# Kernel tuning notes

Measured on AMD Instinct MI355X. Metric: run time of the kernel, lower is better.

The kernel has to match this reference:

```python
import jax, jax.numpy as jnp
import numpy as np

SPATIAL = ((100, 100), (50, 50), (25, 25), (13, 13))
STARTS = [0]
for _h, _w in SPATIAL[:-1]:
    STARTS.append(STARTS[-1] + _h * _w)
L_TOTAL = sum(h * w for h, w in SPATIAL)  # 13294
D, DFFN, NL, NH, NP = 256, 1024, 4, 8, 4
DH = D // NH
EPS = 1e-5


def _ln(x, g, b):
    mu = x.mean(-1, keepdims=True)
    var = ((x - mu) ** 2).mean(-1, keepdims=True)
    return (x - mu) * jax.lax.rsqrt(var + EPS) * g + b


def _bilinear(v_l, x, y, H, W):
    # v_l: [B,NH,H*W,DH]; x,y: [B,NH,Q*NP] pixel coords (grid_sample align_corners=False, zero padding)
    x0f = jnp.floor(x); y0f = jnp.floor(y)
    lx, ly = x - x0f, y - y0f
    x0 = x0f.astype(jnp.int32); y0 = y0f.astype(jnp.int32)
    acc = 0.0
    for dx, dy, w in ((0, 0, (1 - lx) * (1 - ly)), (1, 0, lx * (1 - ly)),
                      (0, 1, (1 - lx) * ly), (1, 1, lx * ly)):
        xi, yi = x0 + dx, y0 + dy
        valid = (xi >= 0) & (xi < W) & (yi >= 0) & (yi < H)
        idx = jnp.clip(yi, 0, H - 1) * W + jnp.clip(xi, 0, W - 1)
        g = jnp.take_along_axis(v_l, idx[..., None], axis=2)  # [B,NH,Q*NP,DH]
        acc = acc + g * (w * valid.astype(w.dtype))[..., None]
    return acc


def _msdeform(query, value_in, ref, norm_wh, Woff, boff, Wattn, battn, Wval, bval, Wout, bout):
    B, Q, _ = query.shape
    v = (value_in @ Wval + bval).reshape(B, L_TOTAL, NH, DH)
    off = (query @ Woff + boff).reshape(B, Q, NH, NL, NP, 2)
    aw = (query @ Wattn + battn).reshape(B, Q, NH, NL * NP)
    aw = jax.nn.softmax(aw, axis=-1).reshape(B, Q, NH, NL, NP)
    # normalized sampling locations in [0,1]: ref + offset / (W,H)
    loc = ref[:, :, None, :, None, :] + off / norm_wh[None, None, None, :, None, :]
    out = 0.0
    for l, (H, W) in enumerate(SPATIAL):
        s = STARTS[l]
        v_l = v[:, s:s + H * W].transpose(0, 2, 1, 3)          # [B,NH,HW,DH]
        loc_l = loc[:, :, :, l].transpose(0, 2, 1, 3, 4)       # [B,NH,Q,NP,2]
        x = (loc_l[..., 0] * W - 0.5).reshape(B, NH, Q * NP)
        y = (loc_l[..., 1] * H - 0.5).reshape(B, NH, Q * NP)
        samp = _bilinear(v_l, x, y, H, W).reshape(B, NH, Q, NP, DH)
        w_l = aw[:, :, :, l].transpose(0, 2, 1, 3)             # [B,NH,Q,NP]
        out = out + (samp * w_l[..., None]).sum(3)             # [B,NH,Q,DH]
    out = out.transpose(0, 2, 1, 3).reshape(B, Q, D)
    return out @ Wout + bout


def setup_inputs() -> dict:
    key = jax.random.key(0)
    ks = jax.random.split(key, 12)
    B = 4
    s = 0.02
    return {
        "src": jax.random.normal(ks[0], (B, L_TOTAL, D), jnp.float32),
        "pos": jax.random.normal(ks[1], (B, L_TOTAL, D), jnp.float32),
        "reference_points": jax.random.uniform(ks[2], (B, L_TOTAL, NL, 2), jnp.float32),
        "spatial_shapes": jnp.array(SPATIAL, jnp.int32),
        "level_start_index": jnp.array(STARTS, jnp.int32),
        "W_off": jax.random.normal(ks[3], (D, NH * NL * NP * 2), jnp.float32) * 0.01,
        "b_off": jax.random.normal(ks[4], (NH * NL * NP * 2,), jnp.float32) * 0.5,
        "W_attn": jax.random.normal(ks[5], (D, NH * NL * NP), jnp.float32) * s,
        "b_attn": jnp.zeros((NH * NL * NP,), jnp.float32),
        "W_val": jax.random.normal(ks[6], (D, D), jnp.float32) * s,
        "b_val": jnp.zeros((D,), jnp.float32),
        "W_out": jax.random.normal(ks[7], (D, D), jnp.float32) * s,
        "b_out": jnp.zeros((D,), jnp.float32),
        "ln_sa_g": jnp.ones((D,), jnp.float32),
        "ln_sa_b": jnp.zeros((D,), jnp.float32),
        "W1": jax.random.normal(ks[8], (D, DFFN), jnp.float32) * s,
        "b1": jnp.zeros((DFFN,), jnp.float32),
        "W2": jax.random.normal(ks[9], (DFFN, D), jnp.float32) * s,
        "b2": jnp.zeros((D,), jnp.float32),
        "ln_ff_g": jnp.ones((D,), jnp.float32),
        "ln_ff_b": jnp.zeros((D,), jnp.float32),
    }


def reference(src, pos, reference_points, spatial_shapes, level_start_index,
              W_off, b_off, W_attn, b_attn, W_val, b_val, W_out, b_out,
              ln_sa_g, ln_sa_b, W1, b1, W2, b2, ln_ff_g, ln_ff_b):
    # offset normalizer is (W, H) per level
    norm_wh = jnp.stack([spatial_shapes[:, 1], spatial_shapes[:, 0]], -1).astype(src.dtype)
    q = src + pos  # with_pos_embed
    sa = _msdeform(q, src, reference_points, norm_wh,
                   W_off, b_off, W_attn, b_attn, W_val, b_val, W_out, b_out)
    x = _ln(sa + src, ln_sa_g, ln_sa_b)          # dropout = identity (eval)
    y = jnp.maximum(x @ W1 + b1, 0.0) @ W2 + b2  # relu FFN
    return _ln(y + x, ln_ff_g, ln_ff_b)
```

## Files before the change

kernel.cpp:

```cpp
#include <hip/hip_runtime.h>
#include <hip/hip_bf16.h>

typedef __hip_bfloat16 bf16;
typedef short bf16x8 __attribute__((ext_vector_type(8)));
typedef float f32x4  __attribute__((ext_vector_type(4)));

#define ROWS 53176
#define LTOT 13294

__device__ __forceinline__ float b2f(bf16 v) { return __bfloat162float(v); }

__device__ __forceinline__ void gl2lds16(const void* g, void* l) {
    __builtin_amdgcn_global_load_lds(
        (const __attribute__((address_space(1))) unsigned*)g,
        (__attribute__((address_space(3))) unsigned*)l, 16, 0, 0);
}

template<bool RELU>
__global__ __launch_bounds__(256)
void mfma_gemm_n(const bf16* __restrict__ A, const bf16* __restrict__ Bt,
                 const float* __restrict__ bias, bf16* __restrict__ C,
                 int M, int N, int K)
{
    __shared__ __align__(16) short As[128 * 32];
    __shared__ __align__(16) short Bs[128 * 32];
    const int tid  = threadIdx.x;
    const int wave = tid >> 6, lane = tid & 63;
    const int m0 = blockIdx.y * 128, n0 = blockIdx.x * 128;
    const int lrow = lane >> 2, lcol = lane & 3;
    const int quad = lane >> 4;

    f32x4 acc[4][4];
#pragma unroll
    for (int i = 0; i < 4; ++i)
#pragma unroll
        for (int j = 0; j < 4; ++j) acc[i][j] = (f32x4){0.f, 0.f, 0.f, 0.f};

    const int wM = (wave >> 1) * 64, wN = (wave & 1) * 64;
    const int foff = (lane & 15) * 32 + quad * 8;

    for (int kk = 0; kk < K; kk += 32) {
#pragma unroll
        for (int q = 0; q < 2; ++q) {
            int rbase = wave * 32 + q * 16;
            int row = rbase + lrow;
            gl2lds16(A  + (size_t)(m0 + row) * K + kk + lcol * 8, &As[rbase * 32]);
            gl2lds16(Bt + (size_t)(n0 + row) * K + kk + lcol * 8, &Bs[rbase * 32]);
        }
        __syncthreads();
        bf16x8 af[4], bfr[4];
#pragma unroll
        for (int i = 0; i < 4; ++i)
            af[i] = *(const bf16x8*)&As[(wM + i * 16) * 32 + foff];
#pragma unroll
        for (int j = 0; j < 4; ++j)
            bfr[j] = *(const bf16x8*)&Bs[(wN + j * 16) * 32 + foff];
#pragma unroll
        for (int i = 0; i < 4; ++i)
#pragma unroll
            for (int j = 0; j < 4; ++j)
                acc[i][j] = __builtin_amdgcn_mfma_f32_16x16x32_bf16(bfr[j], af[i], acc[i][j], 0, 0, 0);
        __syncthreads();
    }

    float4 b4[4];
#pragma unroll
    for (int j = 0; j < 4; ++j)
        b4[j] = *(const float4*)&bias[n0 + wN + j * 16 + quad * 4];

#pragma unroll
    for (int i = 0; i < 4; ++i) {
        int gm = m0 + wM + i * 16 + (lane & 15);
        if (gm >= M) continue;
#pragma unroll
        for (int j = 0; j < 4; ++j) {
            int gn = n0 + wN + j * 16 + quad * 4;
            union { bf16 h[4]; uint2 u2; } pk;
#pragma unroll
            for (int r = 0; r < 4; ++r) {
                float v = acc[i][j][r] + ((const float*)&b4[j])[r];
                if (RELU) v = fmaxf(v, 0.f);
                pk.h[r] = __float2bfloat16(v);
            }
            *(uint2*)&C[(size_t)gm * N + gn] = pk.u2;
        }
    }
}

template<bool RES_BF16, typename OT>
__global__ __launch_bounds__(512)
void mfma_gemm_ln(const bf16* __restrict__ A, const bf16* __restrict__ Bt,
                  const float* __restrict__ bias, const void* __restrict__ res,
                  OT* __restrict__ C, const float* __restrict__ gam,
                  const float* __restrict__ bet, int M, int K)
{
    __shared__ __align__(16) short As[128 * 32];
    __shared__ __align__(16) short Bs[256 * 32];
    __shared__ float rsum[128], rsq[128];
    const int tid  = threadIdx.x;
    const int wave = tid >> 6, lane = tid & 63;
    const int m0 = blockIdx.x * 128;
    const int lrow = lane >> 2, lcol = lane & 3;
    const int quad = lane >> 4;
    if (tid < 128) { rsum[tid] = 0.f; rsq[tid] = 0.f; }

    f32x4 acc[4][4];
#pragma unroll
    for (int i = 0; i < 4; ++i)
#pragma unroll
        for (int j = 0; j < 4; ++j) acc[i][j] = (f32x4){0.f, 0.f, 0.f, 0.f};

    const int wM = (wave >> 2) * 64, wN = (wave & 3) * 64;
    const int foff = (lane & 15) * 32 + quad * 8;

    for (int kk = 0; kk < K; kk += 32) {
#pragma unroll
        for (int q = 0; q < 3; ++q) {
            int r = wave * 48 + q * 16;
            if (r < 128) {
                gl2lds16(A + (size_t)(m0 + r + lrow) * K + kk + lcol * 8, &As[r * 32]);
            } else {
                int rr = r - 128;
                gl2lds16(Bt + (size_t)(rr + lrow) * K + kk + lcol * 8, &Bs[rr * 32]);
            }
        }
        __syncthreads();
        bf16x8 af[4], bfr[4];
#pragma unroll
        for (int i = 0; i < 4; ++i)
            af[i] = *(const bf16x8*)&As[(wM + i * 16) * 32 + foff];
#pragma unroll
        for (int j = 0; j < 4; ++j)
            bfr[j] = *(const bf16x8*)&Bs[(wN + j * 16) * 32 + foff];
#pragma unroll
        for (int i = 0; i < 4; ++i)
#pragma unroll
            for (int j = 0; j < 4; ++j)
                acc[i][j] = __builtin_amdgcn_mfma_f32_16x16x32_bf16(bfr[j], af[i], acc[i][j], 0, 0, 0);
        __syncthreads();
    }

    float4 b4[4], g4[4], be4[4];
#pragma unroll
    for (int j = 0; j < 4; ++j) {
        int gn = wN + j * 16 + quad * 4;
        b4[j]  = *(const float4*)&bias[gn];
        g4[j]  = *(const float4*)&gam[gn];
        be4[j] = *(const float4*)&bet[gn];
    }

    float lsum[4], lsq[4];
#pragma unroll
    for (int i = 0; i < 4; ++i) {
        int gm = m0 + wM + i * 16 + (lane & 15);
        lsum[i] = 0.f; lsq[i] = 0.f;
#pragma unroll
        for (int j = 0; j < 4; ++j) {
            int gn = wN + j * 16 + quad * 4;
            float r4[4] = {0.f, 0.f, 0.f, 0.f};
            if (gm < M) {
                if (RES_BF16) {
                    uint2 ru = *(const uint2*)&((const bf16*)res)[(size_t)gm * 256 + gn];
                    const bf16* rh = (const bf16*)&ru;
#pragma unroll
                    for (int r = 0; r < 4; ++r) r4[r] = b2f(rh[r]);
                } else {
                    float4 rf = *(const float4*)&((const float*)res)[(size_t)gm * 256 + gn];
#pragma unroll
                    for (int r = 0; r < 4; ++r) r4[r] = ((const float*)&rf)[r];
                }
            }
#pragma unroll
            for (int r = 0; r < 4; ++r) {
                float v = acc[i][j][r] + ((const float*)&b4[j])[r] + r4[r];
                acc[i][j][r] = v;
                lsum[i] += v;
                lsq[i]  += v * v;
            }
        }
#pragma unroll
        for (int mask = 16; mask <= 32; mask <<= 1) {
            lsum[i] += __shfl_xor(lsum[i], mask);
            lsq[i]  += __shfl_xor(lsq[i], mask);
        }
    }
    if (quad == 0) {
#pragma unroll
        for (int i = 0; i < 4; ++i) {
            atomicAdd(&rsum[wM + i * 16 + (lane & 15)], lsum[i]);
            atomicAdd(&rsq [wM + i * 16 + (lane & 15)], lsq[i]);
        }
    }
    __syncthreads();

#pragma unroll
    for (int i = 0; i < 4; ++i) {
        int lr = wM + i * 16 + (lane & 15);
        int gm = m0 + lr;
        if (gm >= M) continue;
        float mean = rsum[lr] * (1.f / 256.f);
        float var  = rsq[lr] * (1.f / 256.f) - mean * mean;
        float rstd = rsqrtf(fmaxf(var, 0.f) + 1e-5f);
#pragma unroll
        for (int j = 0; j < 4; ++j) {
            int gn = wN + j * 16 + quad * 4;
            if constexpr (sizeof(OT) == 2) {
                union { bf16 h[4]; uint2 u2; } pk;
#pragma unroll
                for (int r = 0; r < 4; ++r)
                    pk.h[r] = __float2bfloat16((acc[i][j][r] - mean) * rstd *
                              ((const float*)&g4[j])[r] + ((const float*)&be4[j])[r]);
                *(uint2*)&((bf16*)C)[(size_t)gm * 256 + gn] = pk.u2;
            } else {
                float4 o;
#pragma unroll
                for (int r = 0; r < 4; ++r)
                    ((float*)&o)[r] = (acc[i][j][r] - mean) * rstd *
                              ((const float*)&g4[j])[r] + ((const float*)&be4[j])[r];
                *(float4*)&((float*)C)[(size_t)gm * 256 + gn] = o;
            }
        }
    }
}

__global__ void cast_qs_kernel(const float* __restrict__ s, const float* __restrict__ p,
                               bf16* __restrict__ sb, bf16* __restrict__ qb, int n4)
{
    int i = blockIdx.x * 256 + threadIdx.x;
    if (i >= n4) return;
    float4 sv = ((const float4*)s)[i];
    float4 pv = ((const float4*)p)[i];
    union { bf16 h[4]; uint2 u; } a, b;
    a.h[0] = __float2bfloat16(sv.x); a.h[1] = __float2bfloat16(sv.y);
    a.h[2] = __float2bfloat16(sv.z); a.h[3] = __float2bfloat16(sv.w);
    b.h[0] = __float2bfloat16(sv.x + pv.x); b.h[1] = __float2bfloat16(sv.y + pv.y);
    b.h[2] = __float2bfloat16(sv.z + pv.z); b.h[3] = __float2bfloat16(sv.w + pv.w);
    ((uint2*)sb)[i] = a.u;
    ((uint2*)qb)[i] = b.u;
}

__global__ void wt_cast_kernel(const float* __restrict__ W, bf16* __restrict__ Wt, int K, int N)
{
    int e = blockIdx.x * 256 + threadIdx.x;
    if (e >= K * N) return;
    int n = e / K, k = e - n * K;
    Wt[e] = __float2bfloat16(W[(size_t)k * N + n]);
}

__global__ void wcat_cast_kernel(const float* __restrict__ Woff, const float* __restrict__ Wattn,
                                 const float* __restrict__ boff, const float* __restrict__ battn,
                                 bf16* __restrict__ Wt, float* __restrict__ bcat)
{
    int e = blockIdx.x * 256 + threadIdx.x;
    if (e < 384) bcat[e] = (e < 256) ? boff[e] : battn[e - 256];
    if (e >= 384 * 256) return;
    int n = e >> 8, k = e & 255;
    float w = (n < 256) ? Woff[(size_t)k * 256 + n] : Wattn[(size_t)k * 128 + (n - 256)];
    Wt[e] = __float2bfloat16(w);
}

__global__ __launch_bounds__(256)
void sample_kernel(const bf16* __restrict__ v, const bf16* __restrict__ ocat,
                   const float* __restrict__ ref, bf16* __restrict__ samp)
{
    __shared__ int4 tab[16][33];
    const int tid = threadIdx.x;
    const int grp = tid >> 4, lane = tid & 15;
    const int gidx = blockIdx.x * 16 + grp;
    const int h = gidx & 7, bq = gidx >> 3, b = bq / LTOT;

    {
        const int p = lane, l = p >> 2, pp = p & 3;
        const int W = (l == 0) ? 100 : (l == 1) ? 50 : (l == 2) ? 25 : 13;
        const int S = (l == 0) ? 0 : (l == 1) ? 10000 : (l == 2) ? 12500 : 13125;
        const float fW = (float)W;
        float rx = ref[(size_t)bq * 8 + l * 2 + 0];
        float ry = ref[(size_t)bq * 8 + l * 2 + 1];
        const bf16* ob = ocat + (size_t)bq * 384;
        float ox = b2f(ob[h * 32 + l * 8 + pp * 2 + 0]);
        float oy = b2f(ob[h * 32 + l * 8 + pp * 2 + 1]);
        float lg = b2f(ob[256 + h * 16 + p]);
        float m = lg;
#pragma unroll
        for (int mask = 1; mask <= 8; mask <<= 1) m = fmaxf(m, __shfl_xor(m, mask));
        float ev = __expf(lg - m);
        float s = ev;
#pragma unroll
        for (int mask = 1; mask <= 8; mask <<= 1) s += __shfl_xor(s, mask);
        float wgt = ev / s;

        float x = (rx + ox / fW) * fW - 0.5f;
        float y = (ry + oy / fW) * fW - 0.5f;
        float x0f = floorf(x), y0f = floorf(y);
        float lx = x - x0f, ly = y - y0f;
        int x0 = (int)x0f, y0 = (int)y0f;
        float tw[4] = {(1.f - lx) * (1.f - ly), lx * (1.f - ly),
                       (1.f - lx) * ly,         lx * ly};
        const int base = (b * LTOT + S) * 512 + h * 64;
        int  o[4]; float w[4];
#pragma unroll
        for (int t = 0; t < 4; ++t) {
            int xi = x0 + (t & 1), yi = y0 + (t >> 1);
            bool ok = (xi >= 0) & (xi < W) & (yi >= 0) & (yi < W);
            o[t] = ok ? base + (yi * W + xi) * 512 : 0;
            w[t] = ok ? wgt * tw[t] : 0.f;
        }
        tab[grp][p * 2 + 0] = make_int4(o[0], __float_as_int(w[0]), o[1], __float_as_int(w[1]));
        tab[grp][p * 2 + 1] = make_int4(o[2], __float_as_int(w[2]), o[3], __float_as_int(w[3]));
    }
    __syncthreads();

    const int lofs = lane * 4;
    const char* vc = (const char*)v;
    float a0 = 0.f, a1 = 0.f;
#pragma unroll 4
    for (int e2 = 0; e2 < 32; ++e2) {
        int4 q = tab[grp][e2];
        unsigned u0 = *(const unsigned*)(vc + (size_t)(unsigned)(q.x + lofs));
        unsigned u1 = *(const unsigned*)(vc + (size_t)(unsigned)(q.z + lofs));
        float w0 = __int_as_float(q.y), w1 = __int_as_float(q.w);
        a0 += w0 * __uint_as_float(u0 << 16);
        a1 += w0 * __uint_as_float(u0 & 0xffff0000u);
        a0 += w1 * __uint_as_float(u1 << 16);
        a1 += w1 * __uint_as_float(u1 & 0xffff0000u);
    }
    union { struct { bf16 a, b; } h2; unsigned u; } r;
    r.h2.a = __float2bfloat16(a0);
    r.h2.b = __float2bfloat16(a1);
    *(unsigned*)((char*)samp + (size_t)gidx * 64 + lane * 4) = r.u;
}

extern "C" void kernel_launch(void* const* d_in, const int* in_sizes, int n_in,
                              void* d_out, int out_size, void* d_ws, size_t ws_size,
                              hipStream_t stream)
{
    const float* src     = (const float*)d_in[0];
    const float* pos     = (const float*)d_in[1];
    const float* ref     = (const float*)d_in[2];
    const float* W_off   = (const float*)d_in[5];
    const float* b_off   = (const float*)d_in[6];
    const float* W_attn  = (const float*)d_in[7];
    const float* b_attn  = (const float*)d_in[8];
    const float* W_val   = (const float*)d_in[9];
    const float* b_val   = (const float*)d_in[10];
    const float* W_out   = (const float*)d_in[11];
    const float* b_out   = (const float*)d_in[12];
    const float* ln_sa_g = (const float*)d_in[13];
    const float* ln_sa_b = (const float*)d_in[14];
    const float* W1      = (const float*)d_in[15];
    const float* b1      = (const float*)d_in[16];
    const float* W2      = (const float*)d_in[17];
    const float* b2      = (const float*)d_in[18];
    const float* ln_ff_g = (const float*)d_in[19];
    const float* ln_ff_b = (const float*)d_in[20];

    char* ws = (char*)d_ws;
    bf16* sb     = (bf16*)(ws);
    bf16* samp   = (bf16*)(ws);
    bf16* qb     = (bf16*)(ws + 27226112);
    bf16* vbuf   = (bf16*)(ws + 54452224);
    bf16* ocat   = (bf16*)(ws + 81678336);
    bf16* xb16   = (bf16*)(ws + 122517504);
    bf16* hbuf   = (bf16*)(ws);
    bf16* Wval_t = (bf16*)(ws + 149743616);
    bf16* Wcat_t = (bf16*)(ws + 149874688);
    float* bcat  = (float*)(ws + 150071296);
    bf16* Wout_t = (bf16*)(ws + 150072832);
    bf16* W1_t   = (bf16*)(ws + 150203904);
    bf16* W2_t   = (bf16*)(ws + 150728192);
    float* outf  = (float*)d_out;

    dim3 blk(256);

    cast_qs_kernel<<<dim3((ROWS * 64 + 255) / 256), blk, 0, stream>>>(src, pos, sb, qb, ROWS * 64);
    wt_cast_kernel<<<dim3((256 * 256 + 255) / 256),  blk, 0, stream>>>(W_val, Wval_t, 256, 256);
    wcat_cast_kernel<<<dim3((384 * 256 + 255) / 256), blk, 0, stream>>>(W_off, W_attn, b_off, b_attn, Wcat_t, bcat);
    wt_cast_kernel<<<dim3((256 * 256 + 255) / 256),  blk, 0, stream>>>(W_out, Wout_t, 256, 256);
    wt_cast_kernel<<<dim3((256 * 1024 + 255) / 256), blk, 0, stream>>>(W1, W1_t, 256, 1024);
    wt_cast_kernel<<<dim3((1024 * 256 + 255) / 256), blk, 0, stream>>>(W2, W2_t, 1024, 256);

    mfma_gemm_n<false><<<dim3(2, 416), blk, 0, stream>>>(sb, Wval_t, b_val, vbuf, ROWS, 256, 256);
    mfma_gemm_n<false><<<dim3(3, 416), blk, 0, stream>>>(qb, Wcat_t, bcat, ocat, ROWS, 384, 256);
    sample_kernel<<<dim3(ROWS * 8 / 16), blk, 0, stream>>>(vbuf, ocat, ref, samp);
    mfma_gemm_ln<false, bf16><<<dim3(416), dim3(512), 0, stream>>>(
        samp, Wout_t, b_out, src, xb16, ln_sa_g, ln_sa_b, ROWS, 256);
    mfma_gemm_n<true><<<dim3(8, 416), blk, 0, stream>>>(xb16, W1_t, b1, hbuf, ROWS, 1024, 256);
    mfma_gemm_ln<true, float><<<dim3(416), dim3(512), 0, stream>>>(
        hbuf, W2_t, b2, xb16, outf, ln_ff_g, ln_ff_b, ROWS, 1024);
}
```

Measured before the change: 510.1 us.

## Fuse FFN up/down projections with LayerNorm, keeping hidden activations on-chip

```diff
diff --git a/kernel.cpp b/kernel.cpp
--- a/kernel.cpp
+++ b/kernel.cpp
@@ -87,11 +87,10 @@
     }
 }
 
-template<bool RES_BF16, typename OT>
 __global__ __launch_bounds__(512)
 void mfma_gemm_ln(const bf16* __restrict__ A, const bf16* __restrict__ Bt,
-                  const float* __restrict__ bias, const void* __restrict__ res,
-                  OT* __restrict__ C, const float* __restrict__ gam,
+                  const float* __restrict__ bias, const bf16* __restrict__ res,
+                  bf16* __restrict__ C, const float* __restrict__ gam,
                   const float* __restrict__ bet, int M, int K)
 {
     __shared__ __align__(16) short As[128 * 32];
@@ -159,16 +158,10 @@
             int gn = wN + j * 16 + quad * 4;
             float r4[4] = {0.f, 0.f, 0.f, 0.f};
             if (gm < M) {
-                if (RES_BF16) {
-                    uint2 ru = *(const uint2*)&((const bf16*)res)[(size_t)gm * 256 + gn];
-                    const bf16* rh = (const bf16*)&ru;
-#pragma unroll
-                    for (int r = 0; r < 4; ++r) r4[r] = b2f(rh[r]);
-                } else {
-                    float4 rf = *(const float4*)&((const float*)res)[(size_t)gm * 256 + gn];
-#pragma unroll
-                    for (int r = 0; r < 4; ++r) r4[r] = ((const float*)&rf)[r];
-                }
+                uint2 ru = *(const uint2*)&res[(size_t)gm * 256 + gn];
+                const bf16* rh = (const bf16*)&ru;
+#pragma unroll
+                for (int r = 0; r < 4; ++r) r4[r] = b2f(rh[r]);
             }
 #pragma unroll
             for (int r = 0; r < 4; ++r) {
@@ -204,21 +197,173 @@
 #pragma unroll
         for (int j = 0; j < 4; ++j) {
             int gn = wN + j * 16 + quad * 4;
-            if constexpr (sizeof(OT) == 2) {
-                union { bf16 h[4]; uint2 u2; } pk;
+            union { bf16 h[4]; uint2 u2; } pk;
+#pragma unroll
+            for (int r = 0; r < 4; ++r)
+                pk.h[r] = __float2bfloat16((acc[i][j][r] - mean) * rstd *
+                          ((const float*)&g4[j])[r] + ((const float*)&be4[j])[r]);
+            *(uint2*)&C[(size_t)gm * 256 + gn] = pk.u2;
+        }
+    }
+}
+
+__global__ __launch_bounds__(256)
+void ffn_fused(const bf16* __restrict__ x, const bf16* __restrict__ W1t,
+               const float* __restrict__ b1, const bf16* __restrict__ W2t,
+               const float* __restrict__ b2v, float* __restrict__ out,
+               const float* __restrict__ gam, const float* __restrict__ bet, int M)
+{
+    __shared__ __align__(16) short Xs[64 * 264];
+    __shared__ __align__(16) short Hs[64 * 136];
+    __shared__ __align__(16) short Bs[256 * 32];
+    __shared__ float rsum[64], rsq[64];
+    const int tid = threadIdx.x, wave = tid >> 6, lane = tid & 63;
+    const int quad = lane >> 4;
+    const int lrow = lane >> 2, lcol = lane & 3;
+    const int m0 = blockIdx.x * 64;
+    const int foff = (lane & 15) * 32 + quad * 8;
+    if (tid < 64) { rsum[tid] = 0.f; rsq[tid] = 0.f; }
+
+    for (int c = tid; c < 64 * 32; c += 256) {
+        int r = c >> 5, cc = c & 31;
+        int gr = m0 + r; if (gr >= M) gr = M - 1;
+        int4 d = *(const int4*)(x + (size_t)gr * 256 + cc * 8);
+        *(int4*)&Xs[r * 264 + cc * 8] = d;
+    }
+
+    f32x4 acc2[2][8];
+#pragma unroll
+    for (int i = 0; i < 2; ++i)
+#pragma unroll
+        for (int j = 0; j < 8; ++j) acc2[i][j] = (f32x4){0.f, 0.f, 0.f, 0.f};
+
+    const int wM = (wave >> 1) * 32;
+    const int wN1 = (wave & 1) * 64;
+    const int wN2 = (wave & 1) * 128;
+
+    for (int j = 0; j < 8; ++j) {
+        f32x4 acc1[2][4];
+#pragma unroll
+        for (int i = 0; i < 2; ++i)
+#pragma unroll
+            for (int jj = 0; jj < 4; ++jj) acc1[i][jj] = (f32x4){0.f, 0.f, 0.f, 0.f};
+        for (int kk = 0; kk < 256; kk += 32) {
+            __syncthreads();
+#pragma unroll
+            for (int q = 0; q < 2; ++q) {
+                int rbase = wave * 32 + q * 16;
+                gl2lds16(W1t + (size_t)(j * 128 + rbase + lrow) * 256 + kk + lcol * 8,
+                         &Bs[rbase * 32]);
+            }
+            __syncthreads();
+            bf16x8 hf[2], wf[4];
+#pragma unroll
+            for (int i = 0; i < 2; ++i)
+                hf[i] = *(const bf16x8*)&Xs[(wM + i * 16 + (lane & 15)) * 264 + kk + quad * 8];
+#pragma unroll
+            for (int jj = 0; jj < 4; ++jj)
+                wf[jj] = *(const bf16x8*)&Bs[(wN1 + jj * 16) * 32 + foff];
+#pragma unroll
+            for (int i = 0; i < 2; ++i)
+#pragma unroll
+                for (int jj = 0; jj < 4; ++jj)
+                    acc1[i][jj] = __builtin_amdgcn_mfma_f32_16x16x32_bf16(wf[jj], hf[i], acc1[i][jj], 0, 0, 0);
+        }
+#pragma unroll
+        for (int i = 0; i < 2; ++i) {
+            int m = wM + i * 16 + (lane & 15);
+#pragma unroll
+            for (int jj = 0; jj < 4; ++jj) {
+                int n = wN1 + jj * 16 + quad * 4;
+                float4 bb = *(const float4*)&b1[j * 128 + n];
+                union { bf16 h[4]; uint2 u; } pk;
 #pragma unroll
                 for (int r = 0; r < 4; ++r)
-                    pk.h[r] = __float2bfloat16((acc[i][j][r] - mean) * rstd *
-                              ((const float*)&g4[j])[r] + ((const float*)&be4[j])[r]);
-                *(uint2*)&((bf16*)C)[(size_t)gm * 256 + gn] = pk.u2;
-            } else {
-                float4 o;
-#pragma unroll
-                for (int r = 0; r < 4; ++r)
-                    ((float*)&o)[r] = (acc[i][j][r] - mean) * rstd *
-                              ((const float*)&g4[j])[r] + ((const float*)&be4[j])[r];
-                *(float4*)&((float*)C)[(size_t)gm * 256 + gn] = o;
-            }
+                    pk.h[r] = __float2bfloat16(fmaxf(acc1[i][jj][r] + ((const float*)&bb)[r], 0.f));
+                *(uint2*)&Hs[m * 136 + n] = pk.u;
+            }
+        }
+        for (int kk = 0; kk < 128; kk += 32) {
+            __syncthreads();
+#pragma unroll
+            for (int q = 0; q < 4; ++q) {
+                int rbase = wave * 64 + q * 16;
+                gl2lds16(W2t + (size_t)(rbase + lrow) * 1024 + j * 128 + kk + lcol * 8,
+                         &Bs[rbase * 32]);
+            }
+            __syncthreads();
+            bf16x8 hf2[2], wf2[8];
+#pragma unroll
+            for (int i = 0; i < 2; ++i)
+                hf2[i] = *(const bf16x8*)&Hs[(wM + i * 16 + (lane & 15)) * 136 + kk + quad * 8];
+#pragma unroll
+            for (int jj = 0; jj < 8; ++jj)
+                wf2[jj] = *(const bf16x8*)&Bs[(wN2 + jj * 16) * 32 + foff];
+#pragma unroll
+            for (int i = 0; i < 2; ++i)
+#pragma unroll
+                for (int jj = 0; jj < 8; ++jj)
+                    acc2[i][jj] = __builtin_amdgcn_mfma_f32_16x16x32_bf16(wf2[jj], hf2[i], acc2[i][jj], 0, 0, 0);
+        }
+    }
+
+    float4 bb[8], gg[8], be[8];
+#pragma unroll
+    for (int jj = 0; jj < 8; ++jj) {
+        int gn = wN2 + jj * 16 + quad * 4;
+        bb[jj] = *(const float4*)&b2v[gn];
+        gg[jj] = *(const float4*)&gam[gn];
+        be[jj] = *(const float4*)&bet[gn];
+    }
+    float lsum[2], lsq[2];
+#pragma unroll
+    for (int i = 0; i < 2; ++i) {
+        int lr = wM + i * 16 + (lane & 15);
+        lsum[i] = 0.f; lsq[i] = 0.f;
+#pragma unroll
+        for (int jj = 0; jj < 8; ++jj) {
+            int gn = wN2 + jj * 16 + quad * 4;
+            uint2 ru = *(const uint2*)&Xs[lr * 264 + gn];
+            const bf16* rh = (const bf16*)&ru;
+#pragma unroll
+            for (int r = 0; r < 4; ++r) {
+                float v = acc2[i][jj][r] + ((const float*)&bb[jj])[r] + b2f(rh[r]);
+                acc2[i][jj][r] = v;
+                lsum[i] += v;
+                lsq[i]  += v * v;
+            }
+        }
+#pragma unroll
+        for (int mask = 16; mask <= 32; mask <<= 1) {
+            lsum[i] += __shfl_xor(lsum[i], mask);
+            lsq[i]  += __shfl_xor(lsq[i], mask);
+        }
+    }
+    if (quad == 0) {
+#pragma unroll
+        for (int i = 0; i < 2; ++i) {
+            atomicAdd(&rsum[wM + i * 16 + (lane & 15)], lsum[i]);
+            atomicAdd(&rsq [wM + i * 16 + (lane & 15)], lsq[i]);
+        }
+    }
+    __syncthreads();
+#pragma unroll
+    for (int i = 0; i < 2; ++i) {
+        int lr = wM + i * 16 + (lane & 15);
+        int gm = m0 + lr;
+        if (gm >= M) continue;
+        float mean = rsum[lr] * (1.f / 256.f);
+        float var  = rsq[lr] * (1.f / 256.f) - mean * mean;
+        float rstd = rsqrtf(fmaxf(var, 0.f) + 1e-5f);
+#pragma unroll
+        for (int jj = 0; jj < 8; ++jj) {
+            int gn = wN2 + jj * 16 + quad * 4;
+            float4 o;
+#pragma unroll
+            for (int r = 0; r < 4; ++r)
+                ((float*)&o)[r] = (acc2[i][jj][r] - mean) * rstd *
+                        ((const float*)&gg[jj])[r] + ((const float*)&be[jj])[r];
+            *(float4*)&out[(size_t)gm * 256 + gn] = o;
         }
     }
 }
@@ -239,24 +384,33 @@
     ((uint2*)qb)[i] = b.u;
 }
 
-__global__ void wt_cast_kernel(const float* __restrict__ W, bf16* __restrict__ Wt, int K, int N)
-{
-    int e = blockIdx.x * 256 + threadIdx.x;
-    if (e >= K * N) return;
-    int n = e / K, k = e - n * K;
-    Wt[e] = __float2bfloat16(W[(size_t)k * N + n]);
-}
-
-__global__ void wcat_cast_kernel(const float* __restrict__ Woff, const float* __restrict__ Wattn,
-                                 const float* __restrict__ boff, const float* __restrict__ battn,
-                                 bf16* __restrict__ Wt, float* __restrict__ bcat)
+__global__ void wcast_all(const float* __restrict__ Wval, const float* __restrict__ Woff,
+                          const float* __restrict__ Wattn, const float* __restrict__ Wout,
+                          const float* __restrict__ W1, const float* __restrict__ W2,
+                          const float* __restrict__ boff, const float* __restrict__ battn,
+                          bf16* __restrict__ Wval_t, bf16* __restrict__ Wcat_t,
+                          bf16* __restrict__ Wout_t, bf16* __restrict__ W1_t,
+                          bf16* __restrict__ W2_t, float* __restrict__ bcat)
 {
     int e = blockIdx.x * 256 + threadIdx.x;
     if (e < 384) bcat[e] = (e < 256) ? boff[e] : battn[e - 256];
-    if (e >= 384 * 256) return;
-    int n = e >> 8, k = e & 255;
-    float w = (n < 256) ? Woff[(size_t)k * 256 + n] : Wattn[(size_t)k * 128 + (n - 256)];
-    Wt[e] = __float2bfloat16(w);
+    if (e < 65536) {
+        int n = e >> 8, k = e & 255;
+        Wval_t[e] = __float2bfloat16(Wval[k * 256 + n]);
+    } else if (e < 163840) {
+        int i = e - 65536; int n = i >> 8, k = i & 255;
+        float w = (n < 256) ? Woff[k * 256 + n] : Wattn[k * 128 + (n - 256)];
+        Wcat_t[i] = __float2bfloat16(w);
+    } else if (e < 229376) {
+        int i = e - 163840; int n = i >> 8, k = i & 255;
+        Wout_t[i] = __float2bfloat16(Wout[k * 256 + n]);
+    } else if (e < 491520) {
+        int i = e - 229376; int n = i >> 8, k = i & 255;
+        W1_t[i] = __float2bfloat16(W1[k * 1024 + n]);
+    } else if (e < 753664) {
+        int i = e - 491520; int n = i >> 10, k = i & 1023;
+        W2_t[i] = __float2bfloat16(W2[k * 256 + n]);
+    }
 }
 
 __global__ __launch_bounds__(256)
@@ -356,12 +510,11 @@
 
     char* ws = (char*)d_ws;
     bf16* sb     = (bf16*)(ws);
-    bf16* samp   = (bf16*)(ws);
     bf16* qb     = (bf16*)(ws + 27226112);
+    bf16* samp   = (bf16*)(ws + 27226112);
     bf16* vbuf   = (bf16*)(ws + 54452224);
     bf16* ocat   = (bf16*)(ws + 81678336);
     bf16* xb16   = (bf16*)(ws + 122517504);
-    bf16* hbuf   = (bf16*)(ws);
     bf16* Wval_t = (bf16*)(ws + 149743616);
     bf16* Wcat_t = (bf16*)(ws + 149874688);
     float* bcat  = (float*)(ws + 150071296);
@@ -373,18 +526,15 @@
     dim3 blk(256);
 
     cast_qs_kernel<<<dim3((ROWS * 64 + 255) / 256), blk, 0, stream>>>(src, pos, sb, qb, ROWS * 64);
-    wt_cast_kernel<<<dim3((256 * 256 + 255) / 256),  blk, 0, stream>>>(W_val, Wval_t, 256, 256);
-    wcat_cast_kernel<<<dim3((384 * 256 + 255) / 256), blk, 0, stream>>>(W_off, W_attn, b_off, b_attn, Wcat_t, bcat);
-    wt_cast_kernel<<<dim3((256 * 256 + 255) / 256),  blk, 0, stream>>>(W_out, Wout_t, 256, 256);
-    wt_cast_kernel<<<dim3((256 * 1024 + 255) / 256), blk, 0, stream>>>(W1, W1_t, 256, 1024);
-    wt_cast_kernel<<<dim3((1024 * 256 + 255) / 256), blk, 0, stream>>>(W2, W2_t, 1024, 256);
+    wcast_all<<<dim3(2944), blk, 0, stream>>>(W_val, W_off, W_attn, W_out, W1, W2,
+                                              b_off, b_attn,
+                                              Wval_t, Wcat_t, Wout_t, W1_t, W2_t, bcat);
 
     mfma_gemm_n<false><<<dim3(2, 416), blk, 0, stream>>>(sb, Wval_t, b_val, vbuf, ROWS, 256, 256);
     mfma_gemm_n<false><<<dim3(3, 416), blk, 0, stream>>>(qb, Wcat_t, bcat, ocat, ROWS, 384, 256);
     sample_kernel<<<dim3(ROWS * 8 / 16), blk, 0, stream>>>(vbuf, ocat, ref, samp);
-    mfma_gemm_ln<false, bf16><<<dim3(416), dim3(512), 0, stream>>>(
-        samp, Wout_t, b_out, src, xb16, ln_sa_g, ln_sa_b, ROWS, 256);
-    mfma_gemm_n<true><<<dim3(8, 416), blk, 0, stream>>>(xb16, W1_t, b1, hbuf, ROWS, 1024, 256);
-    mfma_gemm_ln<true, float><<<dim3(416), dim3(512), 0, stream>>>(
-        hbuf, W2_t, b2, xb16, outf, ln_ff_g, ln_ff_b, ROWS, 1024);
-}
+    mfma_gemm_ln<<<dim3(416), dim3(512), 0, stream>>>(
+        samp, Wout_t, b_out, sb, xb16, ln_sa_g, ln_sa_b, ROWS, 256);
+    ffn_fused<<<dim3(831), blk, 0, stream>>>(
+        xb16, W1_t, b1, W2_t, b2, outf, ln_ff_g, ln_ff_b, ROWS);
+}
```

After: 562.0 us. +10.2%, slower.
